# Optimization experiments

Measured on AMD Instinct MI355X. Metric: run time of the kernel, lower is better.

The kernel has to match this reference:

```python
import jax, jax.numpy as jnp
import numpy as np

N = 100000      # input points
NS = 12500      # sampled points (fps ratio=0.125)
E = 400000      # edges (~32 neighbors per sampled point)
F_IN = 64       # down_conv_nn[0]
HID = 32        # in_features // 2 (pre_mlp output, PointKernel width)
F_OUT = 128     # down_conv_nn[1]
K = 16          # num kernel points
RADIUS = 1.0
KP_EXTENT = RADIUS / 1.5


def setup_inputs() -> dict:
    key = jax.random.key(0)
    ks = jax.random.split(key, 14)
    x = jax.random.normal(ks[0], (N, F_IN), dtype=jnp.float32)
    pos = jax.random.uniform(ks[1], (N, 3), dtype=jnp.float32, minval=-1.0, maxval=1.0)
    idx = jnp.sort(jax.random.randint(ks[2], (NS,), 0, N))
    edge_src = jax.random.randint(ks[3], (E,), 0, N)    # col: source / full cloud
    edge_dst = jax.random.randint(ks[4], (E,), 0, NS)   # row: target / sampled cloud
    # kernel point positions (stand-in for kernel_point_optimization_debug output)
    kernel = jax.random.uniform(ks[5], (K, 3), dtype=jnp.float32, minval=-RADIUS, maxval=RADIUS)
    # per-kernel-point weight matrices
    kernel_weight = jax.random.normal(ks[6], (K, HID, HID), dtype=jnp.float32) * (1.0 / np.sqrt(HID))
    pre_W = jax.random.normal(ks[7], (F_IN, HID), dtype=jnp.float32) * (1.0 / np.sqrt(F_IN))
    pre_b = jax.random.normal(ks[8], (HID,), dtype=jnp.float32) * 0.01
    post_W = jax.random.normal(ks[9], (HID, F_OUT), dtype=jnp.float32) * (1.0 / np.sqrt(HID))
    post_b = jax.random.normal(ks[10], (F_OUT,), dtype=jnp.float32) * 0.01
    short_W = jax.random.normal(ks[11], (F_IN, F_OUT), dtype=jnp.float32) * (1.0 / np.sqrt(F_IN))
    short_b = jax.random.normal(ks[12], (F_OUT,), dtype=jnp.float32) * 0.01
    return {
        "x": x, "pos": pos,
        "pre_W": pre_W, "pre_b": pre_b,
        "kernel": kernel, "kernel_weight": kernel_weight,
        "post_W": post_W, "post_b": post_b,
        "short_W": short_W, "short_b": short_b,
        "idx": idx, "edge_src": edge_src, "edge_dst": edge_dst,
    }


def reference(x, pos, pre_W, pre_b, kernel, kernel_weight,
              post_W, post_b, short_W, short_b,
              idx, edge_src, edge_dst):
    # pre MLP on full cloud features
    x_side = x @ pre_W + pre_b                      # [N, HID]
    pos_sub = pos[idx]                              # [NS, 3]

    # message: per-edge relative position
    neighbors = pos[edge_src] - pos_sub[edge_dst]   # [E, 3]
    differences = neighbors[:, None, :] - kernel[None, :, :]  # [E, K, 3]
    sq_distances = jnp.sum(differences * differences, axis=-1)  # [E, K]

    # linear KP influence, clipped at 0
    all_weights = jnp.maximum(1.0 - sq_distances / (KP_EXTENT ** 2), 0.0)
    nn1 = jnp.argmin(sq_distances, axis=-1)         # [E] nearest kernel point
    w = jnp.take_along_axis(all_weights, nn1[:, None], axis=1)  # [E, 1]

    K_weights = kernel_weight[nn1]                  # [E, HID, HID] big gather
    weighted_features = w * x_side[edge_src]        # einsum('nb,nc->nc') with b==1
    msg = jnp.einsum('na,nac->nc', weighted_features, K_weights)  # [E, HID]

    # scatter-add aggregation over target nodes
    agg = jax.ops.segment_sum(msg, edge_dst, num_segments=NS)      # [NS, HID]

    out_side = agg @ post_W + post_b                # [NS, F_OUT]
    out_short = x[idx] @ short_W + short_b          # [NS, F_OUT]
    return out_side + out_short
```

## Files before the change

kernel.cpp:

```cpp
#include <hip/hip_runtime.h>

#define F_IN   64
#define HID    32
#define F_OUT  128
#define KPTS   16
#define CAP    80
#define INV_EXT2 2.25f

__global__ __launch_bounds__(256) void k1_pre(
    const float* __restrict__ x, const float* __restrict__ pre_W,
    const float* __restrict__ pre_b, const float* __restrict__ pos,
    const int* __restrict__ idx,
    float* __restrict__ x_side, float* __restrict__ pos_sub,
    int* __restrict__ cursor, uint2* __restrict__ pkw,
    int N, int NS)
{
    const int gt = blockIdx.x * 256 + threadIdx.x;
    const int gstride = gridDim.x * 256;

    for (int i = gt; i < NS; i += gstride) cursor[i] = 0;
    const int PKWN = NS * CAP + 16;
    for (int i = gt; i < PKWN; i += gstride) pkw[i] = make_uint2(0u, 0u);
    for (int i = gt; i < NS * 3; i += gstride) {
        int r = i / 3, c = i - r * 3;
        pos_sub[i] = pos[(long long)idx[r] * 3 + c];
    }

    const int c = threadIdx.x & 31;
    float wcol[F_IN];
#pragma unroll
    for (int a = 0; a < F_IN; ++a) wcol[a] = pre_W[a * HID + c];
    const float bias = pre_b[c];

    const int group   = blockIdx.x * 8 + (threadIdx.x >> 5);
    const int ngroups = gridDim.x * 8;
    for (int row = group; row < N; row += ngroups) {
        const float4* xr = (const float4*)(x + (long long)row * F_IN);
        float acc = bias;
#pragma unroll
        for (int q = 0; q < 16; ++q) {
            const float4 xv = xr[q];
            acc = fmaf(xv.x, wcol[4 * q + 0], acc);
            acc = fmaf(xv.y, wcol[4 * q + 1], acc);
            acc = fmaf(xv.z, wcol[4 * q + 2], acc);
            acc = fmaf(xv.w, wcol[4 * q + 3], acc);
        }
        x_side[(long long)row * HID + c] = acc;
    }
}

__global__ __launch_bounds__(256) void k2_prep(
    const float* __restrict__ pos, const float* __restrict__ pos_sub,
    const float* __restrict__ kp,
    const int* __restrict__ edge_src, const int* __restrict__ edge_dst,
    int* __restrict__ cursor, uint2* __restrict__ pkw, int E)
{
    __shared__ float skp[KPTS * 3];
    if (threadIdx.x < KPTS * 3) skp[threadIdx.x] = kp[threadIdx.x];
    __syncthreads();

    for (int t = blockIdx.x * 256 + threadIdx.x; t < E; t += gridDim.x * 256) {
        const int src = edge_src[t];
        const int dst = edge_dst[t];
        const float nx = pos[src * 3 + 0] - pos_sub[dst * 3 + 0];
        const float ny = pos[src * 3 + 1] - pos_sub[dst * 3 + 1];
        const float nz = pos[src * 3 + 2] - pos_sub[dst * 3 + 2];

        float best = 1e30f;
        int   nn   = 0;
#pragma unroll
        for (int k = 0; k < KPTS; ++k) {
            const float dx = nx - skp[k * 3 + 0];
            const float dy = ny - skp[k * 3 + 1];
            const float dz = nz - skp[k * 3 + 2];
            const float sq = dx * dx + dy * dy + dz * dz;
            if (sq < best) { best = sq; nn = k; }
        }
        const float w = fmaxf(1.0f - best * INV_EXT2, 0.0f);

        const int slot = atomicAdd(&cursor[dst], 1);
        if (slot < CAP)
            pkw[dst * CAP + slot] =
                make_uint2((unsigned)src | ((unsigned)nn << 20), __float_as_uint(w));
    }
}

__global__ __launch_bounds__(512, 4) void k3_agg(
    const uint2* __restrict__ pkw, const int* __restrict__ cursor,
    const float* __restrict__ x_side, const float4* __restrict__ kw4,
    float* __restrict__ agg, int NS)
{
    __shared__ float4 sKW4[KPTS * 256];
    for (int i4 = threadIdx.x; i4 < KPTS * 256; i4 += 512) {
        const int a = (i4 >> 3) & 31;
        const int j = i4 & 7;
        sKW4[(i4 & ~7) | (j ^ (a & 7))] = kw4[i4];
    }
    __syncthreads();

    const int l = threadIdx.x & 31;
    const int g = threadIdx.x >> 5;

    for (int d = blockIdx.x * 16 + g; d < NS; d += gridDim.x * 16) {
        int cnt = cursor[d];
        if (cnt > CAP) cnt = CAP;
        const uint2* bp = pkw + (long long)d * CAP;

        float pacc[32];
#pragma unroll
        for (int k = 0; k < 32; ++k) pacc[k] = 0.0f;

        uint2 a0 = bp[0];
        uint2 a1 = bp[1];
        float xs0 = x_side[(a0.x & 0xFFFFFu) * HID + l];

        for (int i = 0; i < cnt; ++i) {
            const uint2 cur = a0;
            const float xs  = xs0;
            a0 = a1;
            a1 = bp[i + 2];
            xs0 = x_side[(a0.x & 0xFFFFFu) * HID + l];

            const float wf = __uint_as_float(cur.y) * xs;
            const int   rowbase = (int)(cur.x >> 20) * 256 + l * 8;
#pragma unroll
            for (int j = 0; j < 8; ++j) {
                const float4 v = sKW4[rowbase + (j ^ (l & 7))];
                pacc[4 * j + 0] = fmaf(wf, v.x, pacc[4 * j + 0]);
                pacc[4 * j + 1] = fmaf(wf, v.y, pacc[4 * j + 1]);
                pacc[4 * j + 2] = fmaf(wf, v.z, pacc[4 * j + 2]);
                pacc[4 * j + 3] = fmaf(wf, v.w, pacc[4 * j + 3]);
            }
        }

#pragma unroll
        for (int k = 0; k < 16; ++k) {
            const float send = (l & 16) ? pacc[k] : pacc[k + 16];
            const float recv = __shfl_xor(send, 16, 32);
            pacc[k] = ((l & 16) ? pacc[k + 16] : pacc[k]) + recv;
        }
#pragma unroll
        for (int k = 0; k < 8; ++k) {
            const float send = (l & 8) ? pacc[k] : pacc[k + 8];
            const float recv = __shfl_xor(send, 8, 32);
            pacc[k] = ((l & 8) ? pacc[k + 8] : pacc[k]) + recv;
        }
#pragma unroll
        for (int k = 0; k < 4; ++k) {
            const float send = (l & 4) ? pacc[k] : pacc[k + 4];
            const float recv = __shfl_xor(send, 4, 32);
            pacc[k] = ((l & 4) ? pacc[k + 4] : pacc[k]) + recv;
        }
#pragma unroll
        for (int k = 0; k < 2; ++k) {
            const float send = (l & 2) ? pacc[k] : pacc[k + 2];
            const float recv = __shfl_xor(send, 2, 32);
            pacc[k] = ((l & 2) ? pacc[k + 2] : pacc[k]) + recv;
        }
        {
            const float send = (l & 1) ? pacc[0] : pacc[1];
            const float recv = __shfl_xor(send, 1, 32);
            pacc[0] = ((l & 1) ? pacc[1] : pacc[0]) + recv;
        }
        agg[(long long)d * HID + l] = pacc[0];
    }
}

__global__ __launch_bounds__(128) void k4_out(
    const float* __restrict__ agg,
    const float* __restrict__ post_W, const float* __restrict__ post_b,
    const float* __restrict__ x,
    const float* __restrict__ short_W, const float* __restrict__ short_b,
    const int* __restrict__ idx, float* __restrict__ out, int NS)
{
    const int c = threadIdx.x;
    float pw[HID];
#pragma unroll
    for (int a = 0; a < HID; ++a) pw[a] = post_W[a * F_OUT + c];
    float sw[F_IN];
#pragma unroll
    for (int b = 0; b < F_IN; ++b) sw[b] = short_W[b * F_OUT + c];
    const float bias = post_b[c] + short_b[c];

    for (int r = blockIdx.x; r < NS; r += gridDim.x) {
        const float4* ar = (const float4*)(agg + (long long)r * HID);
        const float4* xr = (const float4*)(x + (long long)idx[r] * F_IN);
        float acc = bias;
#pragma unroll
        for (int q = 0; q < 8; ++q) {
            const float4 v = ar[q];
            acc = fmaf(v.x, pw[4 * q + 0], acc);
            acc = fmaf(v.y, pw[4 * q + 1], acc);
            acc = fmaf(v.z, pw[4 * q + 2], acc);
            acc = fmaf(v.w, pw[4 * q + 3], acc);
        }
#pragma unroll
        for (int q = 0; q < 16; ++q) {
            const float4 v = xr[q];
            acc = fmaf(v.x, sw[4 * q + 0], acc);
            acc = fmaf(v.y, sw[4 * q + 1], acc);
            acc = fmaf(v.z, sw[4 * q + 2], acc);
            acc = fmaf(v.w, sw[4 * q + 3], acc);
        }
        out[(long long)r * F_OUT + c] = acc;
    }
}

extern "C" void kernel_launch(void* const* d_in, const int* in_sizes, int n_in,
                              void* d_out, int out_size, void* d_ws, size_t ws_size,
                              hipStream_t stream)
{
    const float* x        = (const float*)d_in[0];
    const float* pos      = (const float*)d_in[1];
    const float* pre_W    = (const float*)d_in[2];
    const float* pre_b    = (const float*)d_in[3];
    const float* kp       = (const float*)d_in[4];
    const float* kweight  = (const float*)d_in[5];
    const float* post_W   = (const float*)d_in[6];
    const float* post_b   = (const float*)d_in[7];
    const float* short_W  = (const float*)d_in[8];
    const float* short_b  = (const float*)d_in[9];
    const int*   idx      = (const int*)d_in[10];
    const int*   edge_src = (const int*)d_in[11];
    const int*   edge_dst = (const int*)d_in[12];
    float*       out      = (float*)d_out;

    const int N  = in_sizes[0] / F_IN;
    const int NS = in_sizes[10];
    const int E  = in_sizes[11];

    char* ws = (char*)d_ws;
    size_t off = 0;
    auto alloc = [&](size_t bytes) {
        void* p = ws + off;
        off = (off + bytes + 255) & ~(size_t)255;
        return p;
    };
    float* x_side  = (float*) alloc((size_t)N * HID * 4);
    float* pos_sub = (float*) alloc((size_t)NS * 3 * 4);
    int*   cursor  = (int*)   alloc((size_t)NS * 4);
    uint2* pkw     = (uint2*) alloc(((size_t)NS * CAP + 16) * 8);
    float* agg     = (float*) alloc((size_t)NS * HID * 4);

    k1_pre<<<512, 256, 0, stream>>>(x, pre_W, pre_b, pos, idx,
                                    x_side, pos_sub, cursor, pkw, N, NS);
    k2_prep<<<(E + 255) / 256, 256, 0, stream>>>(pos, pos_sub, kp,
                                                 edge_src, edge_dst,
                                                 cursor, pkw, E);
    k3_agg<<<512, 512, 0, stream>>>(pkw, cursor, x_side,
                                    (const float4*)kweight, agg, NS);
    k4_out<<<1024, 128, 0, stream>>>(agg, post_W, post_b, x,
                                     short_W, short_b, idx, out, NS);
}
```

Baseline: 141.5 us.

## Bin edge features per kernel point before applying kernel weights in aggregation

New measurement: 196.7 us. 39.0% more time.

```diff
diff --git a/kernel.cpp b/kernel.cpp
--- a/kernel.cpp
+++ b/kernel.cpp
@@ -5,6 +5,7 @@
 #define F_OUT  128
 #define KPTS   16
 #define CAP    80
+#define NSQ    4
 #define INV_EXT2 2.25f
 
 __global__ __launch_bounds__(256) void k1_pre(
@@ -12,15 +13,12 @@
     const float* __restrict__ pre_b, const float* __restrict__ pos,
     const int* __restrict__ idx,
     float* __restrict__ x_side, float* __restrict__ pos_sub,
-    int* __restrict__ cursor, uint2* __restrict__ pkw,
-    int N, int NS)
+    int* __restrict__ cursor, int N, int NS)
 {
     const int gt = blockIdx.x * 256 + threadIdx.x;
     const int gstride = gridDim.x * 256;
 
     for (int i = gt; i < NS; i += gstride) cursor[i] = 0;
-    const int PKWN = NS * CAP + 16;
-    for (int i = gt; i < PKWN; i += gstride) pkw[i] = make_uint2(0u, 0u);
     for (int i = gt; i < NS * 3; i += gstride) {
         int r = i / 3, c = i - r * 3;
         pos_sub[i] = pos[(long long)idx[r] * 3 + c];
@@ -80,89 +78,142 @@
 
         const int slot = atomicAdd(&cursor[dst], 1);
         if (slot < CAP)
-            pkw[dst * CAP + slot] =
+            pkw[(long long)dst * CAP + slot] =
                 make_uint2((unsigned)src | ((unsigned)nn << 20), __float_as_uint(w));
     }
 }
 
-__global__ __launch_bounds__(512, 4) void k3_agg(
+__global__ __launch_bounds__(256, 2) void k3_agg(
     const uint2* __restrict__ pkw, const int* __restrict__ cursor,
     const float* __restrict__ x_side, const float4* __restrict__ kw4,
-    float* __restrict__ agg, int NS)
-{
-    __shared__ float4 sKW4[KPTS * 256];
-    for (int i4 = threadIdx.x; i4 < KPTS * 256; i4 += 512) {
-        const int a = (i4 >> 3) & 31;
-        const int j = i4 & 7;
-        sKW4[(i4 & ~7) | (j ^ (a & 7))] = kw4[i4];
-    }
-    __syncthreads();
-
+    float* __restrict__ agg, int NS, int N)
+{
+    __shared__ float s_lds[8 * NSQ * KPTS * HID];
     const int l = threadIdx.x & 31;
     const int g = threadIdx.x >> 5;
-
-    for (int d = blockIdx.x * 16 + g; d < NS; d += gridDim.x * 16) {
-        int cnt = cursor[d];
-        if (cnt > CAP) cnt = CAP;
-        const uint2* bp = pkw + (long long)d * CAP;
-
-        float pacc[32];
-#pragma unroll
-        for (int k = 0; k < 32; ++k) pacc[k] = 0.0f;
-
-        uint2 a0 = bp[0];
-        uint2 a1 = bp[1];
-        float xs0 = x_side[(a0.x & 0xFFFFFu) * HID + l];
-
-        for (int i = 0; i < cnt; ++i) {
-            const uint2 cur = a0;
-            const float xs  = xs0;
-            a0 = a1;
-            a1 = bp[i + 2];
-            xs0 = x_side[(a0.x & 0xFFFFFu) * HID + l];
-
-            const float wf = __uint_as_float(cur.y) * xs;
-            const int   rowbase = (int)(cur.x >> 20) * 256 + l * 8;
-#pragma unroll
-            for (int j = 0; j < 8; ++j) {
-                const float4 v = sKW4[rowbase + (j ^ (l & 7))];
-                pacc[4 * j + 0] = fmaf(wf, v.x, pacc[4 * j + 0]);
-                pacc[4 * j + 1] = fmaf(wf, v.y, pacc[4 * j + 1]);
-                pacc[4 * j + 2] = fmaf(wf, v.z, pacc[4 * j + 2]);
-                pacc[4 * j + 3] = fmaf(wf, v.w, pacc[4 * j + 3]);
+    float* sg = s_lds + g * (NSQ * KPTS * HID);
+
+    const int nq = (NS + NSQ - 1) / NSQ;
+    const int q  = blockIdx.x * 8 + g;
+    if (q >= nq) return;
+    const int qb = q * NSQ;
+
+    float4* sg4 = (float4*)sg;
+#pragma unroll
+    for (int i = 0; i < 16; ++i)
+        sg4[i * 32 + l] = make_float4(0.f, 0.f, 0.f, 0.f);
+
+    int cnt[NSQ]; const uint2* bp[NSQ]; int maxc = 0;
+#pragma unroll
+    for (int d = 0; d < NSQ; ++d) {
+        const int dd = qb + d;
+        int c0 = (dd < NS) ? cursor[dd] : 0;
+        if (c0 > CAP) c0 = CAP;
+        cnt[d] = c0; if (c0 > maxc) maxc = c0;
+        bp[d] = pkw + (long long)dd * CAP;
+    }
+
+    uint2 eA[NSQ], eB[NSQ];
+    float xsA[NSQ];
+#pragma unroll
+    for (int d = 0; d < NSQ; ++d) eA[d] = bp[d][0];
+#pragma unroll
+    for (int d = 0; d < NSQ; ++d) eB[d] = bp[d][1];
+#pragma unroll
+    for (int d = 0; d < NSQ; ++d) {
+        unsigned si = eA[d].x & 0xFFFFFu; if (si >= (unsigned)N) si = 0;
+        xsA[d] = x_side[si * HID + l];
+    }
+
+    for (int i = 0; i < maxc; ++i) {
+        uint2 eC[NSQ]; float xsB[NSQ];
+#pragma unroll
+        for (int d = 0; d < NSQ; ++d) eC[d] = bp[d][i + 2];
+#pragma unroll
+        for (int d = 0; d < NSQ; ++d) {
+            unsigned si = eB[d].x & 0xFFFFFu; if (si >= (unsigned)N) si = 0;
+            xsB[d] = x_side[si * HID + l];
+        }
+#pragma unroll
+        for (int d = 0; d < NSQ; ++d) {
+            if (i < cnt[d]) {
+                const float wf = __uint_as_float(eA[d].y) * xsA[d];
+                const int   nn = (int)(eA[d].x >> 20);
+                unsafeAtomicAdd(&sg[(d * KPTS + nn) * HID + l], wf);
             }
         }
-
-#pragma unroll
-        for (int k = 0; k < 16; ++k) {
-            const float send = (l & 16) ? pacc[k] : pacc[k + 16];
+#pragma unroll
+        for (int d = 0; d < NSQ; ++d) { eA[d] = eB[d]; eB[d] = eC[d]; xsA[d] = xsB[d]; }
+    }
+
+    float pacc[NSQ][HID];
+#pragma unroll
+    for (int d = 0; d < NSQ; ++d)
+#pragma unroll
+        for (int c = 0; c < HID; ++c) pacc[d][c] = 0.f;
+
+    const float4* kwl = kw4 + l * 8;
+    float4 cur[8], nxt[8];
+#pragma unroll
+    for (int j = 0; j < 8; ++j) cur[j] = kwl[j];
+
+    for (int k = 0; k < KPTS; ++k) {
+        const int kn = (k + 1 < KPTS) ? (k + 1) : k;
+#pragma unroll
+        for (int j = 0; j < 8; ++j) nxt[j] = kwl[kn * 256 + j];
+
+        float sv[NSQ];
+#pragma unroll
+        for (int d = 0; d < NSQ; ++d) sv[d] = sg[(d * KPTS + k) * HID + l];
+
+#pragma unroll
+        for (int j = 0; j < 8; ++j) {
+            const float4 v = cur[j];
+#pragma unroll
+            for (int d = 0; d < NSQ; ++d) {
+                pacc[d][4 * j + 0] = fmaf(sv[d], v.x, pacc[d][4 * j + 0]);
+                pacc[d][4 * j + 1] = fmaf(sv[d], v.y, pacc[d][4 * j + 1]);
+                pacc[d][4 * j + 2] = fmaf(sv[d], v.z, pacc[d][4 * j + 2]);
+                pacc[d][4 * j + 3] = fmaf(sv[d], v.w, pacc[d][4 * j + 3]);
+            }
+        }
+#pragma unroll
+        for (int j = 0; j < 8; ++j) cur[j] = nxt[j];
+    }
+
+#pragma unroll
+    for (int d = 0; d < NSQ; ++d) {
+        float* p = pacc[d];
+#pragma unroll
+        for (int k2 = 0; k2 < 16; ++k2) {
+            const float send = (l & 16) ? p[k2] : p[k2 + 16];
             const float recv = __shfl_xor(send, 16, 32);
-            pacc[k] = ((l & 16) ? pacc[k + 16] : pacc[k]) + recv;
-        }
-#pragma unroll
-        for (int k = 0; k < 8; ++k) {
-            const float send = (l & 8) ? pacc[k] : pacc[k + 8];
+            p[k2] = ((l & 16) ? p[k2 + 16] : p[k2]) + recv;
+        }
+#pragma unroll
+        for (int k2 = 0; k2 < 8; ++k2) {
+            const float send = (l & 8) ? p[k2] : p[k2 + 8];
             const float recv = __shfl_xor(send, 8, 32);
-            pacc[k] = ((l & 8) ? pacc[k + 8] : pacc[k]) + recv;
-        }
-#pragma unroll
-        for (int k = 0; k < 4; ++k) {
-            const float send = (l & 4) ? pacc[k] : pacc[k + 4];
+            p[k2] = ((l & 8) ? p[k2 + 8] : p[k2]) + recv;
+        }
+#pragma unroll
+        for (int k2 = 0; k2 < 4; ++k2) {
+            const float send = (l & 4) ? p[k2] : p[k2 + 4];
             const float recv = __shfl_xor(send, 4, 32);
-            pacc[k] = ((l & 4) ? pacc[k + 4] : pacc[k]) + recv;
-        }
-#pragma unroll
-        for (int k = 0; k < 2; ++k) {
-            const float send = (l & 2) ? pacc[k] : pacc[k + 2];
+            p[k2] = ((l & 4) ? p[k2 + 4] : p[k2]) + recv;
+        }
+#pragma unroll
+        for (int k2 = 0; k2 < 2; ++k2) {
+            const float send = (l & 2) ? p[k2] : p[k2 + 2];
             const float recv = __shfl_xor(send, 2, 32);
-            pacc[k] = ((l & 2) ? pacc[k + 2] : pacc[k]) + recv;
+            p[k2] = ((l & 2) ? p[k2 + 2] : p[k2]) + recv;
         }
         {
-            const float send = (l & 1) ? pacc[0] : pacc[1];
+            const float send = (l & 1) ? p[0] : p[1];
             const float recv = __shfl_xor(send, 1, 32);
-            pacc[0] = ((l & 1) ? pacc[1] : pacc[0]) + recv;
-        }
-        agg[(long long)d * HID + l] = pacc[0];
+            p[0] = ((l & 1) ? p[1] : p[0]) + recv;
+        }
+        if (qb + d < NS) agg[(long long)(qb + d) * HID + l] = p[0];
     }
 }
 
@@ -239,16 +290,20 @@
     float* x_side  = (float*) alloc((size_t)N * HID * 4);
     float* pos_sub = (float*) alloc((size_t)NS * 3 * 4);
     int*   cursor  = (int*)   alloc((size_t)NS * 4);
-    uint2* pkw     = (uint2*) alloc(((size_t)NS * CAP + 16) * 8);
+    uint2* pkw     = (uint2*) alloc(((size_t)NS * CAP + 32) * 8);
     float* agg     = (float*) alloc((size_t)NS * HID * 4);
 
     k1_pre<<<512, 256, 0, stream>>>(x, pre_W, pre_b, pos, idx,
-                                    x_side, pos_sub, cursor, pkw, N, NS);
+                                    x_side, pos_sub, cursor, N, NS);
     k2_prep<<<(E + 255) / 256, 256, 0, stream>>>(pos, pos_sub, kp,
                                                  edge_src, edge_dst,
                                                  cursor, pkw, E);
-    k3_agg<<<512, 512, 0, stream>>>(pkw, cursor, x_side,
-                                    (const float4*)kweight, agg, NS);
+    {
+        const int nq = (NS + NSQ - 1) / NSQ;
+        const int blocks = (nq + 7) / 8;
+        k3_agg<<<blocks, 256, 0, stream>>>(pkw, cursor, x_side,
+                                           (const float4*)kweight, agg, NS, N);
+    }
     k4_out<<<1024, 128, 0, stream>>>(agg, post_W, post_b, x,
                                      short_W, short_b, idx, out, NS);
 }
```
